# Kernel tuning notes

Measured on AMD Instinct MI355X. Metric: run time of the kernel, lower is better.

Reference implementation:

```python
import jax, jax.numpy as jnp
import numpy as np

B = 64          # graphs in batch
NPG = 9         # nodes per graph (max_atoms = NUM_ATOMS = 9)
N = B * NPG     # total nodes = 576
H = 128         # node_dim == hid_dim
SPEC_LEN = 1801
SPEC_COMP = 100
BOND = 3
ASL = BOND * 9 * 9  # action_space_length = 243


def _linear_init(key, fan_in, fan_out):
    # torch.nn.Linear default init: U(-1/sqrt(fan_in), 1/sqrt(fan_in)); stored as [in, out]
    kw, kb = jax.random.split(key)
    bound = 1.0 / np.sqrt(fan_in)
    W = jax.random.uniform(kw, (fan_in, fan_out), jnp.float32, -bound, bound)
    b = jax.random.uniform(kb, (fan_out,), jnp.float32, -bound, bound)
    return W, b


def setup_inputs() -> dict:
    key = jax.random.key(0)
    ks = jax.random.split(key, 10)
    node_features = jax.random.normal(ks[0], (N, H), jnp.float32)
    specs = jax.random.normal(ks[1], (B, 1, SPEC_LEN), jnp.float32)
    # len_vec[b, i] = 1 iff node i belongs to graph b (contiguous 9-node blocks)
    gid = np.repeat(np.arange(B), NPG)
    len_vec = jnp.asarray((gid[None, :] == np.arange(B)[:, None]).astype(np.float32))
    mask = jnp.zeros((B, ASL), jnp.float32)  # additive action mask (0 = allowed)
    indexmask = jax.random.randint(ks[2], (B, ASL), 0, ASL, dtype=jnp.int32)
    W1, b1 = _linear_init(ks[3], SPEC_LEN, SPEC_LEN // 2)
    W2, b2 = _linear_init(ks[4], SPEC_LEN // 2, SPEC_COMP)
    Wv1, bv1 = _linear_init(ks[5], H + SPEC_COMP, H // 2)
    Wv2, bv2 = _linear_init(ks[6], H // 2, 1)
    Wa2, ba2 = _linear_init(ks[7], 2 * H + SPEC_COMP, H)
    Wf, bf = _linear_init(ks[8], H, BOND)
    return {"node_features": node_features, "specs": specs, "len_vec": len_vec,
            "mask": mask, "indexmask": indexmask,
            "W1": W1, "b1": b1, "W2": W2, "b2": b2,
            "Wv1": Wv1, "bv1": bv1, "Wv2": Wv2, "bv2": bv2,
            "Wa2": Wa2, "ba2": ba2, "Wf": Wf, "bf": bf}


def reference(node_features, specs, len_vec, mask, indexmask,
              W1, b1, W2, b2, Wv1, bv1, Wv2, bv2, Wa2, ba2, Wf, bf):
    relu = jax.nn.relu
    n_total, hdim = node_features.shape
    bsz = specs.shape[0]
    npg = n_total // bsz

    # --- spectrum compression: [B,1801] -> [B,100] ---
    s = relu(specs[:, 0, :] @ W1 + b1)
    s = relu(s @ W2 + b2)

    # --- value head: SumPooling readout + spec -> scalar per graph ---
    readout = node_features.reshape(bsz, npg, hdim).sum(axis=1)
    v = relu(jnp.concatenate([readout, s], axis=-1) @ Wv1 + bv1) @ Wv2 + bv2  # [B,1]

    # --- pairwise action features ---
    # original: apf[i,j] = relu(cat(nf[i], nf[j], canvas[i,j])) then Linear(action_2).
    # relu is elementwise and Linear splits over the concat, so factorize:
    #   apf @ Wa2 = relu(nf)[i] @ Wa2[:H]  +  relu(nf)[j] @ Wa2[H:2H]  +  relu(canvas)[i,j] @ Wa2[2H:]
    # canvas is the block-diagonal scatter of s (s >= 0 so relu(canvas) = canvas).
    gid = jnp.arange(n_total) // npg
    same = gid[:, None] == gid[None, :]          # block-diagonal [N,N]
    nf_r = relu(node_features)
    Ai = nf_r @ Wa2[:hdim]                        # [N,H] per-row (Y2) term
    Bj = nf_r @ Wa2[hdim:2 * hdim]                # [N,H] per-col (X2) term
    D = s @ Wa2[2 * hdim:]                        # [B,H] spec-canvas term
    h = relu(Ai[:, None, :] + Bj[None, :, :]
             + jnp.where(same[:, :, None], D[gid][:, None, :], 0.0) + ba2)  # [N,N,H]

    len_matrix = (len_vec.T @ len_vec)[:, :, None]  # block-diagonal pair mask [N,N,1]
    saf = (h @ Wf + bf) * len_matrix                # [N,N,BOND]

    # --- per-graph action assembly (replaces nonzero()+pad+index_select loop) ---
    # with npg nodes per graph the nonzeros of saf are exactly the diagonal
    # npg x npg blocks, flattened (i, j, bond)-major, npg*npg*BOND == ASL.
    rows = jnp.arange(bsz)[:, None] * npg + jnp.arange(npg)[None, :]   # [B,npg]
    fp = saf[rows[:, :, None], rows[:, None, :], :].reshape(bsz, npg * npg * saf.shape[-1])
    gathered = jnp.take_along_axis(fp, indexmask.astype(jnp.int32), axis=1)
    return jax.nn.softmax(gathered + mask, axis=1), v
```

## Files before the change

### kernel.cpp

```cpp
#include <hip/hip_runtime.h>
#include <math.h>

#define BATCH 64
#define NPG 9
#define N_NODES 576
#define HD 128
#define SPEC_LEN 1801
#define S1DIM 900
#define SCOMP 100
#define ASL 243
#define NT 15
#define KC 17
#define KCH 106
#define KT 1856

__global__ __launch_bounds__(256) void k_prep(const float* __restrict__ specs,
                                              float* __restrict__ sT,
                                              float* __restrict__ s1pre) {
    int bb = blockIdx.x, tid = threadIdx.x;
    if (bb < 29) {
        __shared__ float t[64 * 65];
        int k0 = bb * 64;
        int kk = tid & 63, mq = tid >> 6;
#pragma unroll
        for (int p = 0; p < 16; ++p) {
            int m = p * 4 + mq;
            int k = k0 + kk;
            float v = (k < SPEC_LEN) ? specs[(size_t)m * SPEC_LEN + k] : 0.0f;
            t[kk * 65 + m] = v;
        }
        __syncthreads();
#pragma unroll
        for (int p = 0; p < 16; ++p) {
            int o = p * 256 + tid;
            sT[(size_t)k0 * 64 + o] = t[(o >> 6) * 65 + (o & 63)];
        }
    } else {
        int idx = (bb - 29) * 1024 + tid * 4;
        if (idx < BATCH * S1DIM)
            *(float4*)(s1pre + idx) = make_float4(0.f, 0.f, 0.f, 0.f);
    }
}

__global__ __launch_bounds__(256) void k_main(const float* __restrict__ sT,
                                              const float* __restrict__ W1,
                                              const float* __restrict__ nf,
                                              const float* __restrict__ Wa2,
                                              float* __restrict__ s1pre,
                                              float* __restrict__ AB) {
    int bb = blockIdx.x, tid = threadIdx.x;
    if (bb < NT * KC) {
        __shared__ float w1t[16][64];
        int nt = bb % NT, kc = bb / NT;
        int n0 = nt * 64;
        int lane = tid & 63;
        int wid = __builtin_amdgcn_readfirstlane(tid >> 6);
        int m0 = wid * 16;
        int n = n0 + lane;
        int kb = kc * KCH;
        int klen = min(KCH, SPEC_LEN - kb);
        bool nv = (n < S1DIM);

        float acc[16];
#pragma unroll
        for (int i = 0; i < 16; ++i) acc[i] = 0.0f;

        for (int s = 0; s < 7; ++s) {
#pragma unroll
            for (int p = 0; p < 4; ++p) {
                int e = tid + p * 256;
                int kl = s * 16 + (e >> 6);
                int nn = e & 63;
                float v = 0.0f;
                if (kl < klen && (n0 + nn) < S1DIM)
                    v = W1[(size_t)(kb + kl) * S1DIM + n0 + nn];
                w1t[e >> 6][nn] = v;
            }
            __syncthreads();
            const float* sa_base = sT + (size_t)(kb + s * 16) * 64 + m0;
#pragma unroll
            for (int kk = 0; kk < 16; ++kk) {
                float w = w1t[kk][lane];
                const float* sa = sa_base + kk * 64;
#pragma unroll
                for (int i = 0; i < 16; ++i)
                    acc[i] = fmaf(sa[i], w, acc[i]);
            }
            __syncthreads();
        }
        if (nv) {
#pragma unroll
            for (int i = 0; i < 16; ++i)
                atomicAdd(&s1pre[(size_t)(m0 + i) * S1DIM + n], acc[i]);
        }
    } else {
        __shared__ float snf[256];
        int ib = (bb - NT * KC) * 2;
        snf[tid] = fmaxf(nf[(size_t)ib * HD + tid], 0.0f);
        __syncthreads();
        int c = tid;
        const float* __restrict__ wp = (c < HD) ? (Wa2 + c) : (Wa2 + HD * HD + (c - HD));
        float a0 = 0.f, a1 = 0.f;
#pragma unroll 8
        for (int k = 0; k < HD; ++k) {
            float w = wp[(size_t)k * HD];
            a0 = fmaf(snf[k], w, a0);
            a1 = fmaf(snf[HD + k], w, a1);
        }
        AB[(size_t)ib * 256 + c] = a0;
        AB[(size_t)(ib + 1) * 256 + c] = a1;
    }
}

__global__ __launch_bounds__(256) void k_head(const float* __restrict__ s1pre,
                                              const float* __restrict__ b1,
                                              const float* __restrict__ W2,
                                              const float* __restrict__ b2,
                                              const float* __restrict__ Wa2,
                                              const float* __restrict__ nf,
                                              const float* __restrict__ Wv1,
                                              const float* __restrict__ bv1,
                                              const float* __restrict__ Wv2,
                                              const float* __restrict__ bv2,
                                              const float* __restrict__ ba2,
                                              const float* __restrict__ Wf,
                                              const float* __restrict__ bfb,
                                              const int* __restrict__ indexmask,
                                              const float* __restrict__ mask,
                                              const float* __restrict__ AB,
                                              float* __restrict__ out,
                                              float* __restrict__ vout) {
    int m = blockIdx.x, tid = threadIdx.x;
    __shared__ __align__(16) float s1row[S1DIM];
    __shared__ __align__(16) float sAi[NPG * 132];
    __shared__ __align__(16) float sBj[NPG * 132];
    __shared__ __align__(16) float sWfT[3 * HD];
    __shared__ __align__(16) float srow[SCOMP];
    __shared__ __align__(16) float ro[HD];
    __shared__ __align__(16) float sC[HD];
    __shared__ float fp[ASL];
    __shared__ float red[8];

    for (int e = tid; e < S1DIM; e += 256)
        s1row[e] = fmaxf(s1pre[(size_t)m * S1DIM + e] + b1[e], 0.0f);
    for (int e = tid; e < NPG * 256; e += 256) {
        int i = e >> 8, c = e & 255;
        float v = AB[(size_t)(m * NPG + i) * 256 + c];
        if (c < HD) sAi[i * 132 + c] = v;
        else        sBj[i * 132 + (c - HD)] = v;
    }
    for (int e = tid; e < 3 * HD; e += 256)
        sWfT[(e % 3) * HD + (e / 3)] = Wf[e];
    if (tid >= 128) {
        int h = tid - 128;
        float a = 0.0f;
#pragma unroll
        for (int i = 0; i < NPG; ++i) a += nf[(size_t)(m * NPG + i) * HD + h];
        ro[h] = a;
    }
    __syncthreads();

    if (tid < SCOMP) {
        float a = b2[tid];
        for (int k = 0; k < S1DIM; k += 4) {
            const float4 f = *(const float4*)&s1row[k];
            a = fmaf(f.x, W2[(size_t)(k + 0) * SCOMP + tid], a);
            a = fmaf(f.y, W2[(size_t)(k + 1) * SCOMP + tid], a);
            a = fmaf(f.z, W2[(size_t)(k + 2) * SCOMP + tid], a);
            a = fmaf(f.w, W2[(size_t)(k + 3) * SCOMP + tid], a);
        }
        srow[tid] = fmaxf(a, 0.0f);
    }
    __syncthreads();

    if (tid < HD) {
        float a = 0.0f;
        for (int k = 0; k < SCOMP; ++k)
            a = fmaf(srow[k], Wa2[(size_t)(2 * HD + k) * HD + tid], a);
        sC[tid] = a + ba2[tid];
    } else if (tid < 192) {
        int t = tid - 128;
        float a = bv1[t];
        for (int k = 0; k < HD; ++k) a = fmaf(ro[k], Wv1[(size_t)k * 64 + t], a);
        for (int k = 0; k < SCOMP; ++k) a = fmaf(srow[k], Wv1[(size_t)(HD + k) * 64 + t], a);
        a = fmaxf(a, 0.0f);
        float p = a * Wv2[t];
#pragma unroll
        for (int off = 32; off; off >>= 1) p += __shfl_down(p, off, 64);
        if (tid == 128) vout[m] = p + bv2[0];
    }
    __syncthreads();

    for (int e = tid; e < NPG * HD; e += 256) {
        int i = e >> 7, h = e & 127;
        sAi[i * 132 + h] += sC[h];
    }
    __syncthreads();

    if (tid < ASL) {
        int i = tid / 27;
        int j = (tid / 3) % 9;
        int bo = tid % 3;
        float a = bfb[bo];
        const float* pa = sAi + i * 132;
        const float* pb = sBj + j * 132;
        const float* pw = sWfT + bo * HD;
#pragma unroll 8
        for (int h = 0; h < HD; h += 4) {
            const float4 A = *(const float4*)&pa[h];
            const float4 Bv = *(const float4*)&pb[h];
            const float4 W = *(const float4*)&pw[h];
            a = fmaf(fmaxf(A.x + Bv.x, 0.f), W.x, a);
            a = fmaf(fmaxf(A.y + Bv.y, 0.f), W.y, a);
            a = fmaf(fmaxf(A.z + Bv.z, 0.f), W.z, a);
            a = fmaf(fmaxf(A.w + Bv.w, 0.f), W.w, a);
        }
        fp[tid] = a;
    }
    __syncthreads();

    float g = -INFINITY;
    if (tid < ASL) g = fp[indexmask[(size_t)m * ASL + tid]] + mask[(size_t)m * ASL + tid];
    float mx = g;
#pragma unroll
    for (int off = 32; off; off >>= 1) mx = fmaxf(mx, __shfl_down(mx, off, 64));
    if ((tid & 63) == 0) red[tid >> 6] = mx;
    __syncthreads();
    mx = fmaxf(fmaxf(red[0], red[1]), fmaxf(red[2], red[3]));
    float e = (tid < ASL) ? __expf(g - mx) : 0.0f;
    float sm = e;
#pragma unroll
    for (int off = 32; off; off >>= 1) sm += __shfl_down(sm, off, 64);
    if ((tid & 63) == 0) red[4 + (tid >> 6)] = sm;
    __syncthreads();
    sm = red[4] + red[5] + red[6] + red[7];
    if (tid < ASL) out[(size_t)m * ASL + tid] = e / sm;
}

extern "C" void kernel_launch(void* const* d_in, const int* in_sizes, int n_in,
                              void* d_out, int out_size, void* d_ws, size_t ws_size,
                              hipStream_t stream) {
    (void)in_sizes; (void)n_in; (void)out_size; (void)ws_size;
    const float* nf    = (const float*)d_in[0];
    const float* specs = (const float*)d_in[1];
    const float* mask  = (const float*)d_in[3];
    const int*   idxm  = (const int*)d_in[4];
    const float* W1  = (const float*)d_in[5];
    const float* b1  = (const float*)d_in[6];
    const float* W2  = (const float*)d_in[7];
    const float* b2  = (const float*)d_in[8];
    const float* Wv1 = (const float*)d_in[9];
    const float* bv1 = (const float*)d_in[10];
    const float* Wv2 = (const float*)d_in[11];
    const float* bv2 = (const float*)d_in[12];
    const float* Wa2 = (const float*)d_in[13];
    const float* ba2 = (const float*)d_in[14];
    const float* Wf  = (const float*)d_in[15];
    const float* bfv = (const float*)d_in[16];
    float* out = (float*)d_out;
    float* ws  = (float*)d_ws;

    float* sT    = ws;
    float* s1pre = sT + KT * 64;
    float* AB    = s1pre + BATCH * S1DIM;

    k_prep<<<dim3(29 + 57), dim3(256), 0, stream>>>(specs, sT, s1pre);
    k_main<<<dim3(NT * KC + N_NODES / 2), dim3(256), 0, stream>>>(sT, W1, nf, Wa2, s1pre, AB);
    k_head<<<dim3(BATCH), dim3(256), 0, stream>>>(s1pre, b1, W2, b2, Wa2, nf,
                                                  Wv1, bv1, Wv2, bv2, ba2, Wf, bfv,
                                                  idxm, mask, AB, out, out + BATCH * ASL);
}
```

Baseline: 148.2 us.

## Split spectrum second layer into parallel K-chunked kernel and move node projections to prep

The second spectrum linear layer (900->100), which each of 64 head blocks previously ran serially over all 900 inputs, moves into a new kernel of 576 blocks that each handle a 100-wide K chunk and atomically accumulate into a zeroed buffer. The node-feature projection work moves from the first GEMM kernel into the prep kernel with 4 rows per block. The first GEMM now stages its whole W1 K-tile in shared memory once instead of seven synchronised 16-row steps. This adds a kernel launch and more atomics in exchange for removing a long serial dot-product loop from the head kernel.

```diff
diff --git a/kernel.cpp b/kernel.cpp
--- a/kernel.cpp
+++ b/kernel.cpp
@@ -12,11 +12,15 @@
 #define NT 15
 #define KC 17
 #define KCH 106
+#define KPAD 112
 #define KT 1856
 
 __global__ __launch_bounds__(256) void k_prep(const float* __restrict__ specs,
+                                              const float* __restrict__ nf,
+                                              const float* __restrict__ Wa2,
                                               float* __restrict__ sT,
-                                              float* __restrict__ s1pre) {
+                                              float* __restrict__ zbase,
+                                              float* __restrict__ AB) {
     int bb = blockIdx.x, tid = threadIdx.x;
     if (bb < 29) {
         __shared__ float t[64 * 65];
@@ -35,86 +39,99 @@
             int o = p * 256 + tid;
             sT[(size_t)k0 * 64 + o] = t[(o >> 6) * 65 + (o & 63)];
         }
+    } else if (bb < 92) {
+        int idx = (bb - 29) * 1024 + tid * 4;
+        if (idx < BATCH * S1DIM + BATCH * SCOMP)
+            *(float4*)(zbase + idx) = make_float4(0.f, 0.f, 0.f, 0.f);
     } else {
-        int idx = (bb - 29) * 1024 + tid * 4;
-        if (idx < BATCH * S1DIM)
-            *(float4*)(s1pre + idx) = make_float4(0.f, 0.f, 0.f, 0.f);
-    }
-}
-
-__global__ __launch_bounds__(256) void k_main(const float* __restrict__ sT,
-                                              const float* __restrict__ W1,
-                                              const float* __restrict__ nf,
-                                              const float* __restrict__ Wa2,
-                                              float* __restrict__ s1pre,
-                                              float* __restrict__ AB) {
-    int bb = blockIdx.x, tid = threadIdx.x;
-    if (bb < NT * KC) {
-        __shared__ float w1t[16][64];
-        int nt = bb % NT, kc = bb / NT;
-        int n0 = nt * 64;
-        int lane = tid & 63;
-        int wid = __builtin_amdgcn_readfirstlane(tid >> 6);
-        int m0 = wid * 16;
-        int n = n0 + lane;
-        int kb = kc * KCH;
-        int klen = min(KCH, SPEC_LEN - kb);
-        bool nv = (n < S1DIM);
-
-        float acc[16];
-#pragma unroll
-        for (int i = 0; i < 16; ++i) acc[i] = 0.0f;
-
-        for (int s = 0; s < 7; ++s) {
-#pragma unroll
-            for (int p = 0; p < 4; ++p) {
-                int e = tid + p * 256;
-                int kl = s * 16 + (e >> 6);
-                int nn = e & 63;
-                float v = 0.0f;
-                if (kl < klen && (n0 + nn) < S1DIM)
-                    v = W1[(size_t)(kb + kl) * S1DIM + n0 + nn];
-                w1t[e >> 6][nn] = v;
-            }
-            __syncthreads();
-            const float* sa_base = sT + (size_t)(kb + s * 16) * 64 + m0;
-#pragma unroll
-            for (int kk = 0; kk < 16; ++kk) {
-                float w = w1t[kk][lane];
-                const float* sa = sa_base + kk * 64;
-#pragma unroll
-                for (int i = 0; i < 16; ++i)
-                    acc[i] = fmaf(sa[i], w, acc[i]);
-            }
-            __syncthreads();
-        }
-        if (nv) {
-#pragma unroll
-            for (int i = 0; i < 16; ++i)
-                atomicAdd(&s1pre[(size_t)(m0 + i) * S1DIM + n], acc[i]);
-        }
-    } else {
-        __shared__ float snf[256];
-        int ib = (bb - NT * KC) * 2;
-        snf[tid] = fmaxf(nf[(size_t)ib * HD + tid], 0.0f);
+        __shared__ float snf[4 * HD];
+        int ib = (bb - 92) * 4;
+        snf[tid]       = fmaxf(nf[(size_t)ib * HD + tid], 0.0f);
+        snf[256 + tid] = fmaxf(nf[(size_t)ib * HD + 256 + tid], 0.0f);
         __syncthreads();
         int c = tid;
         const float* __restrict__ wp = (c < HD) ? (Wa2 + c) : (Wa2 + HD * HD + (c - HD));
-        float a0 = 0.f, a1 = 0.f;
-#pragma unroll 8
+        float a0 = 0.f, a1 = 0.f, a2 = 0.f, a3 = 0.f;
+#pragma unroll 16
         for (int k = 0; k < HD; ++k) {
             float w = wp[(size_t)k * HD];
             a0 = fmaf(snf[k], w, a0);
             a1 = fmaf(snf[HD + k], w, a1);
-        }
-        AB[(size_t)ib * 256 + c] = a0;
+            a2 = fmaf(snf[2 * HD + k], w, a2);
+            a3 = fmaf(snf[3 * HD + k], w, a3);
+        }
+        AB[(size_t)(ib + 0) * 256 + c] = a0;
         AB[(size_t)(ib + 1) * 256 + c] = a1;
-    }
-}
-
-__global__ __launch_bounds__(256) void k_head(const float* __restrict__ s1pre,
-                                              const float* __restrict__ b1,
-                                              const float* __restrict__ W2,
+        AB[(size_t)(ib + 2) * 256 + c] = a2;
+        AB[(size_t)(ib + 3) * 256 + c] = a3;
+    }
+}
+
+__global__ __launch_bounds__(256) void k_gemm1(const float* __restrict__ sT,
+                                               const float* __restrict__ W1,
+                                               float* __restrict__ s1pre) {
+    __shared__ float w1t[KPAD][64];
+    int bb = blockIdx.x, tid = threadIdx.x;
+    int nt = bb % NT, kc = bb / NT;
+    int n0 = nt * 64;
+    int kb = kc * KCH;
+    int klen = min(KCH, SPEC_LEN - kb);
+    int lane = tid & 63;
+    int m0 = __builtin_amdgcn_readfirstlane(tid >> 6) * 16;
+
+#pragma unroll 7
+    for (int e = tid; e < KPAD * 64; e += 256) {
+        int kl = e >> 6, nn = e & 63;
+        float v = 0.0f;
+        if (kl < klen && (n0 + nn) < S1DIM)
+            v = W1[(size_t)(kb + kl) * S1DIM + n0 + nn];
+        w1t[kl][nn] = v;
+    }
+    __syncthreads();
+
+    float acc[16];
+#pragma unroll
+    for (int i = 0; i < 16; ++i) acc[i] = 0.0f;
+
+    const float* __restrict__ sp = sT + (size_t)kb * 64 + m0;
+#pragma unroll 4
+    for (int kk = 0; kk < KPAD; ++kk) {
+        float w = w1t[kk][lane];
+        const float* __restrict__ sa = sp + kk * 64;
+#pragma unroll
+        for (int i = 0; i < 16; ++i)
+            acc[i] = fmaf(sa[i], w, acc[i]);
+    }
+
+    int n = n0 + lane;
+    if (n < S1DIM) {
+#pragma unroll
+        for (int i = 0; i < 16; ++i)
+            atomicAdd(&s1pre[(size_t)(m0 + i) * S1DIM + n], acc[i]);
+    }
+}
+
+__global__ __launch_bounds__(128) void k_gemm2(const float* __restrict__ s1pre,
+                                               const float* __restrict__ b1,
+                                               const float* __restrict__ W2,
+                                               float* __restrict__ s1c) {
+    __shared__ float sld[SCOMP];
+    int bb = blockIdx.x, tid = threadIdx.x;
+    int m = bb / 9;
+    int kb = (bb % 9) * 100;
+    if (tid < 100)
+        sld[tid] = fmaxf(s1pre[(size_t)m * S1DIM + kb + tid] + b1[kb + tid], 0.0f);
+    __syncthreads();
+    if (tid < SCOMP) {
+        float a = 0.0f;
+#pragma unroll 10
+        for (int kl = 0; kl < 100; ++kl)
+            a = fmaf(sld[kl], W2[(size_t)(kb + kl) * SCOMP + tid], a);
+        atomicAdd(&s1c[(size_t)m * SCOMP + tid], a);
+    }
+}
+
+__global__ __launch_bounds__(256) void k_head(const float* __restrict__ s1c,
                                               const float* __restrict__ b2,
                                               const float* __restrict__ Wa2,
                                               const float* __restrict__ nf,
@@ -131,18 +148,15 @@
                                               float* __restrict__ out,
                                               float* __restrict__ vout) {
     int m = blockIdx.x, tid = threadIdx.x;
-    __shared__ __align__(16) float s1row[S1DIM];
     __shared__ __align__(16) float sAi[NPG * 132];
     __shared__ __align__(16) float sBj[NPG * 132];
-    __shared__ __align__(16) float sWfT[3 * HD];
+    __shared__ __align__(16) float sWfT[3 * 132];
     __shared__ __align__(16) float srow[SCOMP];
     __shared__ __align__(16) float ro[HD];
     __shared__ __align__(16) float sC[HD];
     __shared__ float fp[ASL];
     __shared__ float red[8];
 
-    for (int e = tid; e < S1DIM; e += 256)
-        s1row[e] = fmaxf(s1pre[(size_t)m * S1DIM + e] + b1[e], 0.0f);
     for (int e = tid; e < NPG * 256; e += 256) {
         int i = e >> 8, c = e & 255;
         float v = AB[(size_t)(m * NPG + i) * 256 + c];
@@ -150,7 +164,9 @@
         else        sBj[i * 132 + (c - HD)] = v;
     }
     for (int e = tid; e < 3 * HD; e += 256)
-        sWfT[(e % 3) * HD + (e / 3)] = Wf[e];
+        sWfT[(e % 3) * 132 + (e / 3)] = Wf[e];
+    if (tid < SCOMP)
+        srow[tid] = fmaxf(s1c[(size_t)m * SCOMP + tid] + b2[tid], 0.0f);
     if (tid >= 128) {
         int h = tid - 128;
         float a = 0.0f;
@@ -160,28 +176,18 @@
     }
     __syncthreads();
 
-    if (tid < SCOMP) {
-        float a = b2[tid];
-        for (int k = 0; k < S1DIM; k += 4) {
-            const float4 f = *(const float4*)&s1row[k];
-            a = fmaf(f.x, W2[(size_t)(k + 0) * SCOMP + tid], a);
-            a = fmaf(f.y, W2[(size_t)(k + 1) * SCOMP + tid], a);
-            a = fmaf(f.z, W2[(size_t)(k + 2) * SCOMP + tid], a);
-            a = fmaf(f.w, W2[(size_t)(k + 3) * SCOMP + tid], a);
-        }
-        srow[tid] = fmaxf(a, 0.0f);
-    }
-    __syncthreads();
-
     if (tid < HD) {
         float a = 0.0f;
+#pragma unroll 10
         for (int k = 0; k < SCOMP; ++k)
             a = fmaf(srow[k], Wa2[(size_t)(2 * HD + k) * HD + tid], a);
         sC[tid] = a + ba2[tid];
     } else if (tid < 192) {
         int t = tid - 128;
         float a = bv1[t];
+#pragma unroll 8
         for (int k = 0; k < HD; ++k) a = fmaf(ro[k], Wv1[(size_t)k * 64 + t], a);
+#pragma unroll 10
         for (int k = 0; k < SCOMP; ++k) a = fmaf(srow[k], Wv1[(size_t)(HD + k) * 64 + t], a);
         a = fmaxf(a, 0.0f);
         float p = a * Wv2[t];
@@ -191,10 +197,8 @@
     }
     __syncthreads();
 
-    for (int e = tid; e < NPG * HD; e += 256) {
-        int i = e >> 7, h = e & 127;
-        sAi[i * 132 + h] += sC[h];
-    }
+    for (int e = tid; e < NPG * HD; e += 256)
+        sAi[(e >> 7) * 132 + (e & 127)] += sC[e & 127];
     __syncthreads();
 
     if (tid < ASL) {
@@ -204,7 +208,7 @@
         float a = bfb[bo];
         const float* pa = sAi + i * 132;
         const float* pb = sBj + j * 132;
-        const float* pw = sWfT + bo * HD;
+        const float* pw = sWfT + bo * 132;
 #pragma unroll 8
         for (int h = 0; h < HD; h += 4) {
             const float4 A = *(const float4*)&pa[h];
@@ -262,11 +266,13 @@
 
     float* sT    = ws;
     float* s1pre = sT + KT * 64;
-    float* AB    = s1pre + BATCH * S1DIM;
-
-    k_prep<<<dim3(29 + 57), dim3(256), 0, stream>>>(specs, sT, s1pre);
-    k_main<<<dim3(NT * KC + N_NODES / 2), dim3(256), 0, stream>>>(sT, W1, nf, Wa2, s1pre, AB);
-    k_head<<<dim3(BATCH), dim3(256), 0, stream>>>(s1pre, b1, W2, b2, Wa2, nf,
+    float* s1c   = s1pre + BATCH * S1DIM;
+    float* AB    = s1c + BATCH * SCOMP;
+
+    k_prep<<<dim3(92 + 144), dim3(256), 0, stream>>>(specs, nf, Wa2, sT, s1pre, AB);
+    k_gemm1<<<dim3(NT * KC), dim3(256), 0, stream>>>(sT, W1, s1pre);
+    k_gemm2<<<dim3(BATCH * 9), dim3(128), 0, stream>>>(s1pre, b1, W2, s1c);
+    k_head<<<dim3(BATCH), dim3(256), 0, stream>>>(s1c, b2, Wa2, nf,
                                                   Wv1, bv1, Wv2, bv2, ba2, Wf, bfv,
                                                   idxm, mask, AB, out, out + BATCH * ASL);
 }
```

Measured after the change: 137.4 us. 7.3% less time.
